# Performance work log

Hardware: AMD Instinct MI355X
Metric: run time of the kernel (lower is better)

Reference implementation:

```python
import jax, jax.numpy as jnp
import numpy as np

# NF4 codebook (bitsandbytes normal-float-4 values)
NF4 = jnp.asarray(np.array([
    -1.0, -0.6961928009986877, -0.5250730514526367, -0.39491748809814453,
    -0.28444138169288635, -0.18477343022823334, -0.09105003625154495, 0.0,
    0.07958029955625534, 0.16093020141124725, 0.24611230194568634, 0.33791524171829224,
    0.44070982933044434, 0.5626170039176941, 0.7229568362236023, 1.0], dtype=np.float32))

BLOCK = 64         # bnb nf4 blocksize
SCALING = 2.0      # alpha / r = 128 / 64
OUT, IN = 4096, 4096

def dequantize_nf4(codes, absmax):
    # codes: [out, in] int32 in [0,16); absmax: [out*in/BLOCK] per-block scale
    vals = NF4[codes].reshape(-1, BLOCK)           # [n_blocks, BLOCK]
    w = vals * absmax[:, None]                     # blockwise rescale
    return w.reshape(OUT, IN)                      # [out, in]

def setup_inputs() -> dict:
    key = jax.random.key(0)
    k1, k2, k3, k4, k5 = jax.random.split(key, 5)
    x = jax.random.normal(k1, (4, 2048, 4096), dtype=jnp.float32)
    lora_A = jax.random.normal(k2, (64, 4096), dtype=jnp.float32) * 0.02
    lora_B = jax.random.normal(k3, (4096, 64), dtype=jnp.float32) * 0.02
    absmax = jax.random.uniform(k4, (4096 * 4096 // BLOCK,), dtype=jnp.float32) * 0.1
    qweight_codes = jax.random.randint(k5, (4096, 4096), 0, 16, dtype=jnp.int32)
    return {"x": x, "lora_A": lora_A, "lora_B": lora_B,
            "absmax": absmax, "qweight_codes": qweight_codes}

def reference(x, lora_A, lora_B, absmax, qweight_codes):
    # LinearForward, quantized nf4 path, no dora/bone, dropout disabled (eval):
    # F.linear(x, W) + scaling * F.linear(F.linear(x, lora_A), lora_B)
    W = dequantize_nf4(qweight_codes, absmax)              # [out, in]
    base = jnp.einsum('btd,od->bto', x, W)                 # base GEMM
    lora = jnp.einsum('btr,or->bto', jnp.einsum('btd,rd->btr', x, lora_A), lora_B)
    return base + SCALING * lora
```

## Files before the change

kernel.cpp:

```cpp
#include <hip/hip_runtime.h>


typedef _Float16 half8 __attribute__((ext_vector_type(8)));
typedef float f32x4 __attribute__((ext_vector_type(4)));

#define M_DIM 8192
#define N_DIM 4096
#define K_DIM 4096
#define NT (K_DIM / 64)

__constant__ float NF4C[16] = {
    -1.0f, -0.6961928009986877f, -0.5250730514526367f, -0.39491748809814453f,
    -0.28444138169288635f, -0.18477343022823334f, -0.09105003625154495f, 0.0f,
    0.07958029955625534f, 0.16093020141124725f, 0.24611230194568634f, 0.33791524171829224f,
    0.44070982933044434f, 0.5626170039176941f, 0.7229568362236023f, 1.0f};

__device__ __forceinline__ void gl16(void* lds_p, const void* g) {
  __builtin_amdgcn_global_load_lds(
      (const __attribute__((address_space(1))) void*)g,
      (__attribute__((address_space(3))) void*)lds_p, 16, 0, 0);
}

__global__ __launch_bounds__(256) void prep_x(const float4* __restrict__ x,
                                              half8* __restrict__ xh) {
  size_t i = (size_t)blockIdx.x * 256 + threadIdx.x;
  float4 a = x[2 * i];
  float4 b = x[2 * i + 1];
  half8 h;
  h[0] = (_Float16)a.x; h[1] = (_Float16)a.y; h[2] = (_Float16)a.z; h[3] = (_Float16)a.w;
  h[4] = (_Float16)b.x; h[5] = (_Float16)b.y; h[6] = (_Float16)b.z; h[7] = (_Float16)b.w;
  xh[i] = h;
}

#define PWP 132
__global__ __launch_bounds__(256) void prep_w(const float* __restrict__ lora_A,
                                              const float* __restrict__ lora_B,
                                              const float* __restrict__ absmax,
                                              const int* __restrict__ codes,
                                              _Float16* __restrict__ Wc) {
  __shared__ float At[64 * PWP];
  __shared__ float Bt[64 * PWP];
  __shared__ float nf4s[16];
  const int tid = threadIdx.x;
  const int bxi = blockIdx.x & 31;
  const int byo = blockIdx.x >> 5;
  const int i0 = bxi * 128;
  const int o0 = byo * 128;
  if (tid < 16) nf4s[tid] = NF4C[tid];
  for (int idx = tid; idx < 8192; idx += 256) {
    int r = idx >> 7, ii = idx & 127;
    At[r * PWP + ii] = lora_A[(size_t)r * 4096 + i0 + ii];
  }
  for (int idx = tid; idx < 8192; idx += 256) {
    int oo = idx >> 6, r = idx & 63;
    Bt[r * PWP + oo] = lora_B[(size_t)(o0 + oo) * 64 + r];
  }
  __syncthreads();
  const int tx = tid & 15;
  const int ty = tid >> 4;
  float accw[8][8];
#pragma unroll
  for (int i = 0; i < 8; ++i)
#pragma unroll
    for (int j = 0; j < 8; ++j) accw[i][j] = 0.0f;
  for (int r = 0; r < 64; ++r) {
    float4 a0 = *(const float4*)&At[r * PWP + tx * 8];
    float4 a1 = *(const float4*)&At[r * PWP + tx * 8 + 4];
    float4 b0 = *(const float4*)&Bt[r * PWP + ty * 8];
    float4 b1 = *(const float4*)&Bt[r * PWP + ty * 8 + 4];
    float av[8] = {a0.x, a0.y, a0.z, a0.w, a1.x, a1.y, a1.z, a1.w};
    float bv[8] = {b0.x, b0.y, b0.z, b0.w, b1.x, b1.y, b1.z, b1.w};
#pragma unroll
    for (int i = 0; i < 8; ++i)
#pragma unroll
      for (int j = 0; j < 8; ++j) accw[i][j] += bv[i] * av[j];
  }
#pragma unroll
  for (int i = 0; i < 8; ++i) {
    const int o_g = o0 + ty * 8 + i;
    const int* crow = codes + (size_t)o_g * 4096 + i0 + tx * 8;
    int4 c0 = *(const int4*)crow;
    int4 c1 = *(const int4*)(crow + 4);
    const float am = absmax[o_g * 64 + (i0 >> 6) + (tx >> 3)];
    half8 h;
    h[0] = (_Float16)(nf4s[c0.x] * am + 2.0f * accw[i][0]);
    h[1] = (_Float16)(nf4s[c0.y] * am + 2.0f * accw[i][1]);
    h[2] = (_Float16)(nf4s[c0.z] * am + 2.0f * accw[i][2]);
    h[3] = (_Float16)(nf4s[c0.w] * am + 2.0f * accw[i][3]);
    h[4] = (_Float16)(nf4s[c1.x] * am + 2.0f * accw[i][4]);
    h[5] = (_Float16)(nf4s[c1.y] * am + 2.0f * accw[i][5]);
    h[6] = (_Float16)(nf4s[c1.z] * am + 2.0f * accw[i][6]);
    h[7] = (_Float16)(nf4s[c1.w] * am + 2.0f * accw[i][7]);
    *(half8*)(Wc + (size_t)o_g * 4096 + i0 + tx * 8) = h;
  }
}


#define BAR __builtin_amdgcn_s_barrier()
#define PRIO1 __builtin_amdgcn_s_setprio(1)
#define PRIO0 __builtin_amdgcn_s_setprio(0)
#define SB0 __builtin_amdgcn_sched_barrier(0)

#define VMC_(N) asm volatile("s_waitcnt vmcnt(" #N ")" ::: "memory")
#define VMC(N) VMC_(N)
#define LG_(N)                                              \
  do {                                                      \
    asm volatile("s_waitcnt lgkmcnt(" #N ")" ::: "memory"); \
    __builtin_amdgcn_sched_barrier(0);                      \
  } while (0)
#define LG(N) LG_(N)

__global__ __launch_bounds__(512, 2) void gemm(const _Float16* __restrict__ Xh,
                                               const _Float16* __restrict__ Wc,
                                               float* __restrict__ out) {
  __shared__ _Float16 lds[65536];
  const int tid = threadIdx.x;
  const int lane = tid & 63;
  const int w = tid >> 6;

  const int swz = (blockIdx.x & 7) * 64 + (blockIdx.x >> 3);
  const int by = swz >> 4;
  const int bx = swz & 15;

  const int m16 = lane & 15;
  const int quad = lane >> 4;
  const int csw = (quad ^ (m16 & 7)) * 8;
  const int aoff0 = m16 * 64 + csw;
  const int aoff1 = m16 * 64 + (csw ^ 32);
  const int ha = w >> 2;
  const int hboff = ((w & 3) >> 1) * 8192 + (w & 1) * 4096;

  const int r0 = tid >> 3;
  const int lc = (tid & 7) ^ (r0 & 7);
  const _Float16* gAbase = Xh + (size_t)(by * 256 + r0) * K_DIM + lc * 8;
  const _Float16* gBbase = Wc + (size_t)(bx * 256 + r0) * K_DIM + lc * 8;

#define STAGE_A(H, BUF, T)                                                \
  do {                                                                    \
    _Float16* d_ = lds + (BUF) * 32768 + (H) * 8192 + w * 512;            \
    const _Float16* s_ = gAbase + (size_t)((H) * 128) * K_DIM + (T) * 64; \
    gl16(d_, s_);                                                         \
    gl16(d_ + 4096, s_ + (size_t)64 * K_DIM);                             \
  } while (0)
#define STAGE_B(H, BUF, T)                                                \
  do {                                                                    \
    _Float16* d_ = lds + (BUF) * 32768 + 16384 + (H) * 8192 + w * 512;    \
    const _Float16* s_ = gBbase + (size_t)((H) * 128) * K_DIM + (T) * 64; \
    gl16(d_, s_);                                                         \
    gl16(d_ + 4096, s_ + (size_t)64 * K_DIM);                             \
  } while (0)

  f32x4 acc[8][4];
#pragma unroll
  for (int m = 0; m < 8; ++m)
#pragma unroll
    for (int n = 0; n < 4; ++n) acc[m][n] = (f32x4){0.f, 0.f, 0.f, 0.f};

  half8 af[4][2];
  half8 bf[2][2];

#define RDA(FM, P)                                          \
  do {                                                      \
    af[FM][0] = *(const half8*)((P) + (FM)*1024 + aoff0);   \
    af[FM][1] = *(const half8*)((P) + (FM)*1024 + aoff1);   \
  } while (0)
#define RDB(FN, P)                                          \
  do {                                                      \
    bf[FN][0] = *(const half8*)((P) + (FN)*1024 + aoff0);   \
    bf[FN][1] = *(const half8*)((P) + (FN)*1024 + aoff1);   \
  } while (0)

#define MFM(FM, MH, NH)                                                      \
  do {                                                                       \
    acc[(MH)*4 + (FM)][(NH)*2 + 0] = __builtin_amdgcn_mfma_f32_16x16x32_f16( \
        af[FM][0], bf[0][0], acc[(MH)*4 + (FM)][(NH)*2 + 0], 0, 0, 0);       \
    acc[(MH)*4 + (FM)][(NH)*2 + 0] = __builtin_amdgcn_mfma_f32_16x16x32_f16( \
        af[FM][1], bf[0][1], acc[(MH)*4 + (FM)][(NH)*2 + 0], 0, 0, 0);       \
    acc[(MH)*4 + (FM)][(NH)*2 + 1] = __builtin_amdgcn_mfma_f32_16x16x32_f16( \
        af[FM][0], bf[1][0], acc[(MH)*4 + (FM)][(NH)*2 + 1], 0, 0, 0);       \
    acc[(MH)*4 + (FM)][(NH)*2 + 1] = __builtin_amdgcn_mfma_f32_16x16x32_f16( \
        af[FM][1], bf[1][1], acc[(MH)*4 + (FM)][(NH)*2 + 1], 0, 0, 0);       \
  } while (0)

#define MFN(FN, MH, NH)                                                          \
  do {                                                                           \
    _Pragma("unroll") for (int fm_ = 0; fm_ < 4; ++fm_) {                        \
      acc[(MH)*4 + fm_][(NH)*2 + (FN)] = __builtin_amdgcn_mfma_f32_16x16x32_f16( \
          af[fm_][0], bf[FN][0], acc[(MH)*4 + fm_][(NH)*2 + (FN)], 0, 0, 0);     \
      acc[(MH)*4 + fm_][(NH)*2 + (FN)] = __builtin_amdgcn_mfma_f32_16x16x32_f16( \
          af[fm_][1], bf[FN][1], acc[(MH)*4 + fm_][(NH)*2 + (FN)], 0, 0, 0);     \
    }                                                                            \
  } while (0)

#define TILE(BUF, T, S1, S4, VW)                                        \
  do {                                                                  \
    const _Float16* rA = lds + (BUF)*32768 + ha * 8192;                 \
    const _Float16* rB = lds + (BUF)*32768 + 16384 + hboff;             \
                                     \
    RDB(0, rB); RDB(1, rB); RDA(0, rA);                                 \
    SB0;                                                                \
    RDA(1, rA); RDA(2, rA); RDA(3, rA);                                 \
    if (S1) {                                                           \
      STAGE_A(1, (BUF) ^ 1, (T) + 1);                                   \
      STAGE_B(0, (BUF) ^ 1, (T) + 1);                                   \
      STAGE_B(1, (BUF) ^ 1, (T) + 1);                                   \
    }                                                                   \
    BAR;                                                                \
    PRIO1;                                                              \
    LG(6); MFM(0, 0, 0);                                                \
    LG(4); MFM(1, 0, 0);                                                \
    LG(2); MFM(2, 0, 0);                                                \
    LG(0); MFM(3, 0, 0);                                                \
    PRIO0;                                                              \
    BAR;                                                                \
                                              \
    RDB(0, rB + 2048);                                                  \
    SB0;                                                                \
    RDB(1, rB + 2048);                                                  \
    BAR;                                                                \
    PRIO1;                                                              \
    LG(2); MFN(0, 0, 1);                                                \
    LG(0); MFN(1, 0, 1);                                                \
    PRIO0;                                                              \
    BAR;                                                                \
                                              \
    RDA(0, rA + 4096);                                                  \
    SB0;                                                                \
    RDA(1, rA + 4096); RDA(2, rA + 4096); RDA(3, rA + 4096);            \
    BAR;                                                                \
    PRIO1;                                                              \
    LG(6); MFM(0, 1, 1);                                                \
    LG(4); MFM(1, 1, 1);                                                \
    LG(2); MFM(2, 1, 1);                                                \
    LG(0); MFM(3, 1, 1);                                                \
    PRIO0;                                                              \
    BAR;                                                                \
     \
    RDB(0, rB);                                                         \
    SB0;                                                                \
    RDB(1, rB);                                                         \
    if (S4) STAGE_A(0, BUF, (T) + 2);                                   \
    BAR;                                                                \
    PRIO1;                                                              \
    LG(2); MFN(0, 1, 0);                                                \
    LG(0); MFN(1, 1, 0);                                                \
    PRIO0;                                                              \
    VMC(VW);                                                            \
    BAR;                                                                \
  } while (0)

  STAGE_A(0, 0, 0);
  STAGE_A(1, 0, 0);
  STAGE_B(0, 0, 0);
  STAGE_B(1, 0, 0);
  STAGE_A(0, 1, 1);
  VMC(2);
  BAR;

  for (int t2 = 0; t2 < NT - 2; t2 += 2) {
    TILE(0, t2, 1, 1, 2);
    TILE(1, t2 + 1, 1, 1, 2);
  }
  TILE(0, NT - 2, 1, 0, 0);
  TILE(1, NT - 1, 0, 0, 0);

  const size_t rowbase = (size_t)by * 256 + ha * 128 + quad * 4;
  const int colbase = bx * 256 + (w & 3) * 64 + m16;
#pragma unroll
  for (int m = 0; m < 8; ++m) {
#pragma unroll
    for (int r = 0; r < 4; ++r) {
      float* po = out + (rowbase + m * 16 + r) * N_DIM + colbase;
      po[0]  = acc[m][0][r];
      po[16] = acc[m][1][r];
      po[32] = acc[m][2][r];
      po[48] = acc[m][3][r];
    }
  }
}

extern "C" void kernel_launch(void* const* d_in, const int* in_sizes, int n_in,
                              void* d_out, int out_size, void* d_ws, size_t ws_size,
                              hipStream_t stream) {
  const float* x      = (const float*)d_in[0];
  const float* lora_A = (const float*)d_in[1];
  const float* lora_B = (const float*)d_in[2];
  const float* absmax = (const float*)d_in[3];
  const int*   codes  = (const int*)d_in[4];
  float* out = (float*)d_out;

  _Float16* Xh = (_Float16*)d_ws;
  _Float16* Wc = Xh + (size_t)M_DIM * K_DIM;

  hipLaunchKernelGGL(prep_x, dim3((M_DIM * K_DIM) / (8 * 256)), dim3(256), 0, stream,
                     (const float4*)x, (half8*)Xh);
  hipLaunchKernelGGL(prep_w, dim3((N_DIM / 128) * (K_DIM / 128)), dim3(256), 0, stream,
                     lora_A, lora_B, absmax, codes, Wc);
  hipLaunchKernelGGL(gemm, dim3((M_DIM / 256) * (N_DIM / 256)), dim3(512), 0, stream,
                     Xh, Wc, out);
}
```

Baseline: 529.1 us.

## Simplify GEMM tile pipeline to a single barrier per K tile

Measured after the change: 534.6 us. About the same (+1.0%).

```diff
diff --git a/kernel.cpp b/kernel.cpp
--- a/kernel.cpp
+++ b/kernel.cpp
@@ -192,60 +192,49 @@
     }                                                                            \
   } while (0)
 
-#define TILE(BUF, T, S1, S4, VW)                                        \
+#define TILE1(BUF, T, S)                                                \
   do {                                                                  \
     const _Float16* rA = lds + (BUF)*32768 + ha * 8192;                 \
     const _Float16* rB = lds + (BUF)*32768 + 16384 + hboff;             \
-                                     \
-    RDB(0, rB); RDB(1, rB); RDA(0, rA);                                 \
-    SB0;                                                                \
-    RDA(1, rA); RDA(2, rA); RDA(3, rA);                                 \
-    if (S1) {                                                           \
+                   \
+    RDB(0, rB); RDB(1, rB);                                             \
+    RDA(0, rA); RDA(1, rA); RDA(2, rA); RDA(3, rA);                     \
+    if (S) {                      \
+      STAGE_A(0, (BUF) ^ 1, (T) + 1);                                   \
       STAGE_A(1, (BUF) ^ 1, (T) + 1);                                   \
       STAGE_B(0, (BUF) ^ 1, (T) + 1);                                   \
       STAGE_B(1, (BUF) ^ 1, (T) + 1);                                   \
     }                                                                   \
-    BAR;                                                                \
-    PRIO1;                                                              \
-    LG(6); MFM(0, 0, 0);                                                \
+     \
+    PRIO1;                                                              \
+    LG(6); MFM(0, 0, 0);                             \
     LG(4); MFM(1, 0, 0);                                                \
     LG(2); MFM(2, 0, 0);                                                \
     LG(0); MFM(3, 0, 0);                                                \
     PRIO0;                                                              \
-    BAR;                                                                \
-                                              \
-    RDB(0, rB + 2048);                                                  \
-    SB0;                                                                \
-    RDB(1, rB + 2048);                                                  \
-    BAR;                                                                \
+       \
+    RDB(0, rB + 2048); RDB(1, rB + 2048);                               \
     PRIO1;                                                              \
     LG(2); MFN(0, 0, 1);                                                \
     LG(0); MFN(1, 0, 1);                                                \
     PRIO0;                                                              \
-    BAR;                                                                \
-                                              \
-    RDA(0, rA + 4096);                                                  \
-    SB0;                                                                \
-    RDA(1, rA + 4096); RDA(2, rA + 4096); RDA(3, rA + 4096);            \
-    BAR;                                                                \
+          \
+    RDA(0, rA + 4096); RDA(1, rA + 4096);                               \
+    RDA(2, rA + 4096); RDA(3, rA + 4096);                               \
     PRIO1;                                                              \
     LG(6); MFM(0, 1, 1);                                                \
     LG(4); MFM(1, 1, 1);                                                \
     LG(2); MFM(2, 1, 1);                                                \
     LG(0); MFM(3, 1, 1);                                                \
     PRIO0;                                                              \
-    BAR;                                                                \
-     \
-    RDB(0, rB);                                                         \
-    SB0;                                                                \
-    RDB(1, rB);                                                         \
-    if (S4) STAGE_A(0, BUF, (T) + 2);                                   \
-    BAR;                                                                \
+        \
+    RDB(0, rB); RDB(1, rB);                                             \
     PRIO1;                                                              \
     LG(2); MFN(0, 1, 0);                                                \
     LG(0); MFN(1, 1, 0);                                                \
     PRIO0;                                                              \
-    VMC(VW);                                                            \
+        \
+    VMC(0);                                                             \
     BAR;                                                                \
   } while (0)
 
@@ -253,16 +242,15 @@
   STAGE_A(1, 0, 0);
   STAGE_B(0, 0, 0);
   STAGE_B(1, 0, 0);
-  STAGE_A(0, 1, 1);
-  VMC(2);
+  VMC(0);
   BAR;
 
   for (int t2 = 0; t2 < NT - 2; t2 += 2) {
-    TILE(0, t2, 1, 1, 2);
-    TILE(1, t2 + 1, 1, 1, 2);
-  }
-  TILE(0, NT - 2, 1, 0, 0);
-  TILE(1, NT - 1, 0, 0, 0);
+    TILE1(0, t2, 1);
+    TILE1(1, t2 + 1, 1);
+  }
+  TILE1(0, NT - 2, 1);
+  TILE1(1, NT - 1, 0);
 
   const size_t rowbase = (size_t)by * 256 + ha * 128 + quad * 4;
   const int colbase = bx * 256 + (w & 3) * 64 + m16;
```
